# Kernel tuning notes

Hardware: AMD Instinct MI355X
Metric: run time of the kernel (lower is better)

## Reference

```python
import jax, jax.numpy as jnp
import numpy as np

HEADS, DIM_HEAD = 8, 64  # per init_kwargs


def cdist(x, w):
    """Euclidean distance between rows of x [..., n, d] and w [m, d] -> [..., n, m].
    Matches torch.cdist (non-squared) / L2DistanceLinear(squared=False)."""
    sq = (x * x).sum(-1, keepdims=True) + (w * w).sum(-1) - 2.0 * (x @ w.T)
    return jnp.sqrt(jnp.maximum(sq, 0.0))


def setup_inputs() -> dict:
    key = jax.random.key(0)
    k1, k2, k3 = jax.random.split(key, 3)
    B, N, D = 4, 2048, 512
    dim_inner = HEADS * DIM_HEAD  # 512
    x = jax.random.normal(k1, (B, N, D), dtype=jnp.float32)
    w_qkv = jax.random.normal(k2, (3 * dim_inner, D), dtype=jnp.float32)
    w_out = jax.random.normal(k3, (D, dim_inner), dtype=jnp.float32)
    return {"x": x, "w_qkv": w_qkv, "w_out": w_out}


def reference(x, w_qkv, w_out):
    B, N, D = x.shape
    scale = DIM_HEAD ** -0.5

    # L2-distance QKV projection (cdist, non-squared, no negate/bias)
    qkv = cdist(x, w_qkv)                                  # [B, N, 3*H*DH]
    qkv = qkv.reshape(B, N, 3, HEADS, DIM_HEAD).transpose(2, 0, 3, 1, 4)  # [3, B, H, N, DH]
    q, k, v = qkv[0], qkv[1], qkv[2]

    # neg squared-L2 attention scores: -(||q||^2 + ||k||^2 - 2 q.k)
    q_sq = (q * q).sum(-1)                                 # [B, H, N]
    k_sq = (k * k).sum(-1)                                 # [B, H, N]
    dots = jnp.einsum('bhid,bhjd->bhij', q, k)             # [B, H, N, N]
    sim = -(q_sq[..., :, None] + k_sq[..., None, :] - 2.0 * dots) * scale

    attn = jax.nn.softmax(sim, axis=-1)
    out = jnp.einsum('bhij,bhjd->bhid', attn, v)           # [B, H, N, DH]
    out = out.transpose(0, 2, 1, 3).reshape(B, N, HEADS * DIM_HEAD)

    # L2-distance output projection
    return cdist(out, w_out)                               # [B, N, D]
```

## Files before the change

kernel.cpp:

```cpp
#include <hip/hip_runtime.h>
#include <stdint.h>

typedef float v4f  __attribute__((ext_vector_type(4)));
typedef float v16f __attribute__((ext_vector_type(16)));
typedef short v8s  __attribute__((ext_vector_type(8)));
typedef uint32_t u32;

#define DEVI static __device__ __forceinline__

DEVI unsigned short f2bf(float f) {
    u32 u = __builtin_bit_cast(u32, f);
    u = (u + 0x7fffu + ((u >> 16) & 1u)) >> 16;
    return (unsigned short)u;
}
DEVI float bf2f(unsigned short h) {
    u32 u = ((u32)h) << 16;
    return __builtin_bit_cast(float, u);
}

DEVI float fexp2(float x) {
#if __has_builtin(__builtin_amdgcn_exp2f)
    return __builtin_amdgcn_exp2f(x);
#else
    float r;
    asm("v_exp_f32 %0, %1" : "=v"(r) : "v"(x));
    return r;
#endif
}

template <typename T>
DEVI void async16(const T* g, T* l) {
    __builtin_amdgcn_global_load_lds(
        (const __attribute__((address_space(1))) u32*)g,
        (__attribute__((address_space(3))) u32*)l, 16, 0, 0);
}

DEVI v4f bmfma(v8s a, v8s b, v4f c) {
    return __builtin_amdgcn_mfma_f32_16x16x32_bf16(a, b, c, 0, 0, 0);
}
DEVI v16f bmfma32(v8s a, v8s b, v16f c) {
    return __builtin_amdgcn_mfma_f32_32x32x16_bf16(a, b, c, 0, 0, 0);
}

#if __has_builtin(__builtin_amdgcn_permlane32_swap)
#define HAVE_PLSWAP 1
typedef unsigned int v2u __attribute__((ext_vector_type(2)));
#endif

DEVI void swap32(u32 a, u32 b, u32& lo, u32& hi) {
#ifdef HAVE_PLSWAP
    v2u r = __builtin_amdgcn_permlane32_swap(a, b, false, false);
    lo = r.x; hi = r.y;
#else
    u32 ax = __shfl_xor(a, 32), bx = __shfl_xor(b, 32);
    int hh = (threadIdx.x & 63) >> 5;
    lo = hh ? bx : a;
    hi = hh ? b : ax;
#endif
}

static const size_t HSZ = 32ull * 2048 * 64;

__launch_bounds__(256, 2)
__global__ void prep_all(const float* __restrict__ X, const float* __restrict__ WQ,
                         const float* __restrict__ WO,
                         unsigned short* __restrict__ Xb, unsigned short* __restrict__ WQb,
                         unsigned short* __restrict__ WOb,
                         float* __restrict__ xsq, float* __restrict__ wqsq,
                         float* __restrict__ wosq, float* __restrict__ wors)
{
    const int bid = blockIdx.x;
    const int w = threadIdx.x >> 6, lane = threadIdx.x & 63;
    const float* src; unsigned short* dst; float* Sq; float* Rs = nullptr;
    int r;
    if (bid < 2048)      { src = X;  dst = Xb;  Sq = xsq;  r = bid * 4 + w; }
    else if (bid < 2432) { src = WQ; dst = WQb; Sq = wqsq; r = (bid - 2048) * 4 + w; }
    else                 { src = WO; dst = WOb; Sq = wosq; Rs = wors; r = (bid - 2432) * 4 + w; }

    const float* xr = src + (size_t)r * 512 + lane * 8;
    float4 a = *(const float4*)xr;
    float4 c = *(const float4*)(xr + 4);
    float s = a.x*a.x + a.y*a.y + a.z*a.z + a.w*a.w
            + c.x*c.x + c.y*c.y + c.z*c.z + c.w*c.w;
    float sm = a.x + a.y + a.z + a.w + c.x + c.y + c.z + c.w;
    uint4 pkv;
    unsigned short* e = (unsigned short*)&pkv;
    e[0] = f2bf(a.x); e[1] = f2bf(a.y); e[2] = f2bf(a.z); e[3] = f2bf(a.w);
    e[4] = f2bf(c.x); e[5] = f2bf(c.y); e[6] = f2bf(c.z); e[7] = f2bf(c.w);
    *(uint4*)(dst + (size_t)r * 512 + lane * 8) = pkv;
#pragma unroll
    for (int d = 32; d > 0; d >>= 1) {
        s  += __shfl_xor(s, d);
        sm += __shfl_xor(sm, d);
    }
    if (lane == 0) { Sq[r] = s; if (Rs) Rs[r] = sm; }
}

__launch_bounds__(256, 2)
__global__ void gemm_cdist(const unsigned short* __restrict__ A,
                           const unsigned short* __restrict__ B,
                           const float* __restrict__ Asq,
                           const float* __restrict__ Bsq,
                           unsigned short* __restrict__ QKV,
                           float* __restrict__ Ksqc)
{
    __shared__ unsigned short lsm[4 * 8192];
    const int t = threadIdx.x;
    const int lane = t & 63, w = t >> 6;
    const int low = lane & 15, quad = lane >> 4;
    const int wm = w & 1, wn = w >> 1;
    const int tM = blockIdx.x * 128, tN = blockIdx.y * 128;

    v4f acc[4][4];
#pragma unroll
    for (int a = 0; a < 4; ++a)
#pragma unroll
        for (int b = 0; b < 4; ++b) acc[a][b] = (v4f){0.f, 0.f, 0.f, 0.f};

    int kstage = 0;
    auto STAGE = [&](int buf) {
        unsigned short* lA = lsm + buf * 8192;
        unsigned short* lB = lA + 4096;
#pragma unroll
        for (int is = 0; is < 2; ++is) {
            int slot = is * 256 + t;
            int r = slot >> 2, bp = slot & 3, bs = bp ^ (r & 3);
            async16(A + (size_t)(tM + r) * 512 + kstage + bs * 8, lA + slot * 8);
            async16(B + (size_t)(tN + r) * 512 + kstage + bs * 8, lB + slot * 8);
        }
        kstage += 32;
    };

    STAGE(0);
    STAGE(1);

#pragma unroll
    for (int iter = 0; iter < 16; ++iter) {
        if (iter <= 13) STAGE((iter + 2) & 3);
        if (iter <= 13)      asm volatile("s_waitcnt vmcnt(8)" ::: "memory");
        else if (iter == 14) asm volatile("s_waitcnt vmcnt(4)" ::: "memory");
        else                 asm volatile("s_waitcnt vmcnt(0)" ::: "memory");
        __builtin_amdgcn_s_barrier();
        __builtin_amdgcn_sched_barrier(0);

        const unsigned short* lA = lsm + (iter & 3) * 8192;
        const unsigned short* lB = lA + 4096;

        v8s bfr[4];
#pragma unroll
        for (int ns = 0; ns < 4; ++ns) {
            int row = wn * 64 + ns * 16 + low;
            bfr[ns] = *(const v8s*)(lB + (row * 4 + (quad ^ (row & 3))) * 8);
        }
#pragma unroll
        for (int ms = 0; ms < 4; ++ms) {
            int row = wm * 64 + ms * 16 + low;
            v8s af = *(const v8s*)(lA + (row * 4 + (quad ^ (row & 3))) * 8);
#pragma unroll
            for (int ns = 0; ns < 4; ++ns)
                acc[ms][ns] = bmfma(af, bfr[ns], acc[ms][ns]);
        }
    }

    const int tt = tN >> 9;
    if (tt != 2) {
#pragma unroll
        for (int ms = 0; ms < 4; ++ms) {
#pragma unroll
            for (int reg = 0; reg < 4; ++reg) {
                const int row = tM + wm * 64 + ms * 16 + quad * 4 + reg;
                const int b = row >> 11, i = row & 2047;
                float kacc = 0.f;
#pragma unroll
                for (int ns = 0; ns < 4; ++ns) {
                    const int col = tN + wn * 64 + ns * 16 + low;
                    float dot = acc[ms][ns][reg];
                    float val = sqrtf(fmaxf(Asq[row] + Bsq[col] - 2.f * dot, 0.f)) - 32.f;
                    int h = (col >> 6) & 7, d = col & 63, bh = b * 8 + h;
                    if (tt == 0) {
                        QKV[((size_t)bh * 2048 + i) * 64 + d] =
                            f2bf(val * 0.36067376022224085f);
                    } else {
                        QKV[HSZ + ((size_t)bh * 2048 + i) * 64 + d] = f2bf(val);
                        kacc += val * val;
                    }
                }
                if (tt == 1) {
#pragma unroll
                    for (int d = 1; d < 16; d <<= 1) kacc += __shfl_xor(kacc, d);
                    if (low == 0) {
                        int h = ((tN + wn * 64) >> 6) & 7;
                        Ksqc[(size_t)(b * 8 + h) * 2048 + i] = -kacc * 0.18033688011112042f;
                    }
                }
            }
        }
    } else {
        u32 packed[4][4][2];
#pragma unroll
        for (int ms = 0; ms < 4; ++ms)
#pragma unroll
            for (int ns = 0; ns < 4; ++ns) {
                const int col = tN + wn * 64 + ns * 16 + low;
                float bs_ = Bsq[col];
#pragma unroll
                for (int rp = 0; rp < 2; ++rp) {
                    u32 pk = 0;
#pragma unroll
                    for (int sub = 0; sub < 2; ++sub) {
                        int reg = rp * 2 + sub;
                        int row = tM + wm * 64 + ms * 16 + quad * 4 + reg;
                        float val = sqrtf(fmaxf(Asq[row] + bs_
                                                - 2.f * acc[ms][ns][reg], 0.f)) - 32.f;
                        pk |= (u32)f2bf(val) << (16 * sub);
                    }
                    packed[ms][ns][rp] = pk;
                }
            }
        u32* lT32 = (u32*)lsm;
#pragma unroll
        for (int p = 0; p < 2; ++p) {
            __syncthreads();
            if (wm == p) {
#pragma unroll
                for (int ms = 0; ms < 4; ++ms)
#pragma unroll
                    for (int ns = 0; ns < 4; ++ns) {
                        int cl = wn * 64 + ns * 16 + low;
#pragma unroll
                        for (int rp = 0; rp < 2; ++rp)
                            lT32[cl * 36 + ms * 8 + quad * 2 + rp] = packed[ms][ns][rp];
                    }
            }
            __syncthreads();
#pragma unroll
            for (int cc = 0; cc < 4; ++cc) {
                int col = cc * 32 + (t >> 3);
                int i0 = (t & 7) * 8;
                uint4 vvv = *(const uint4*)(lsm + col * 72 + i0);
                int colg = tN + col;
                int h = (colg >> 6) & 7, d = colg & 63;
                int rowg = tM + p * 64 + i0;
                int b = rowg >> 11, i = rowg & 2047;
                *(uint4*)(QKV + 2 * HSZ
                          + ((size_t)((b * 8 + h) * 64 + d)) * 2048 + i) = vvv;
            }
        }
    }
    (void)0;
}

__launch_bounds__(256, 2)
__global__ void flash_attn(const unsigned short* __restrict__ Q,
                           const unsigned short* __restrict__ K,
                           const unsigned short* __restrict__ VT,
                           const float* __restrict__ Ksqc,
                           unsigned short* __restrict__ OP,
                           float* __restrict__ Osqp)
{
    __shared__ unsigned short lK[4][64 * 64];
    __shared__ unsigned short lV[4][64 * 64];
    __shared__ float lKqA[2048];
    const int t = threadIdx.x, lane = t & 63, w = t >> 6;
    const int i31 = lane & 31, h = lane >> 5;
    const int bid = blockIdx.x;
    const int bh = (bid & 7) * 4 + (bid >> 7);
    const int qt = (bid >> 3) & 15;
    const size_t base = (size_t)bh * (2048 * 64);
    const int row0 = qt * 128 + w * 32;

    v8s qfr[4];
#pragma unroll
    for (int kt = 0; kt < 4; ++kt)
        qfr[kt] = *(const v8s*)(Q + base + (size_t)(row0 + i31) * 64 + kt * 16 + h * 8);

    v16f o[2];
    float lacc = 0.f;
#pragma unroll
    for (int dt = 0; dt < 2; ++dt)
#pragma unroll
        for (int r = 0; r < 16; ++r) o[dt][r] = 0.f;

    const unsigned short* kg = K + base;
    const unsigned short* vg = VT + (size_t)bh * 64 * 2048;
    const float* kqg = Ksqc + (size_t)bh * 2048;

    auto STAGE = [&](int buf) {
#pragma unroll
        for (int is = 0; is < 2; ++is) {
            int slot = is * 256 + t;
            int r = slot >> 3, bp = slot & 7, bs = bp ^ (r & 7);
            async16(kg + (size_t)r * 64 + bs * 8, &lK[buf][slot * 8]);
        }
#pragma unroll
        for (int is = 0; is < 2; ++is) {
            int slot = is * 256 + t;
            int r = slot >> 3, bp = slot & 7, bs = bp ^ (r & 7);
            async16(vg + (size_t)r * 2048 + bs * 8, &lV[buf][slot * 8]);
        }
        kg += 64 * 64; vg += 64;
    };

    auto COMPUTE = [&](int cb, int kqoff) {
        const int jrow0 = i31, jrow1 = 32 + i31;
        v8s kf0[4], kf1[4];
#pragma unroll
        for (int kt = 0; kt < 4; ++kt) {
            kf0[kt] = *(const v8s*)(&lK[cb][(jrow0 * 8 + ((2 * kt + h) ^ (jrow0 & 7))) * 8]);
            kf1[kt] = *(const v8s*)(&lK[cb][(jrow1 * 8 + ((2 * kt + h) ^ (jrow1 & 7))) * 8]);
        }
        v16f sa0, sa1;
#pragma unroll
        for (int r1 = 0; r1 < 4; ++r1) {
            v4f kq0 = *(const v4f*)(&lKqA[kqoff + r1 * 8 + h * 4]);
            v4f kq1 = *(const v4f*)(&lKqA[kqoff + 32 + r1 * 8 + h * 4]);
#pragma unroll
            for (int u = 0; u < 4; ++u) {
                sa0[4 * r1 + u] = kq0[u];
                sa1[4 * r1 + u] = kq1[u];
            }
        }
#pragma unroll
        for (int kt = 0; kt < 4; ++kt) sa0 = bmfma32(kf0[kt], qfr[kt], sa0);
#pragma unroll
        for (int kt = 0; kt < 4; ++kt) sa1 = bmfma32(kf1[kt], qfr[kt], sa1);

        u32 pk0[8];
#pragma unroll
        for (int r1 = 0; r1 < 4; ++r1) {
            float p0 = fexp2(sa0[4 * r1 + 0]);
            float p1 = fexp2(sa0[4 * r1 + 1]);
            float p2 = fexp2(sa0[4 * r1 + 2]);
            float p3 = fexp2(sa0[4 * r1 + 3]);
            lacc += (p0 + p1) + (p2 + p3);
            pk0[2 * r1] = __builtin_amdgcn_perm(
                __builtin_bit_cast(u32, p1), __builtin_bit_cast(u32, p0),
                0x07060302u);
            pk0[2 * r1 + 1] = __builtin_amdgcn_perm(
                __builtin_bit_cast(u32, p3), __builtin_bit_cast(u32, p2),
                0x07060302u);
        }
#pragma unroll
        for (int c2 = 0; c2 < 2; ++c2) {
            const int jb = 2 * c2;
            v8s vf[2];
#pragma unroll
            for (int dt = 0; dt < 2; ++dt) {
                const int drow = dt * 32 + i31;
                vf[dt] = *(const v8s*)(&lV[cb][(drow * 8 + ((jb + h) ^ (drow & 7))) * 8]);
            }
            uint4 dd;
            swap32(pk0[4 * c2 + 0], pk0[4 * c2 + 2], dd.x, dd.z);
            swap32(pk0[4 * c2 + 1], pk0[4 * c2 + 3], dd.y, dd.w);
            v8s af = __builtin_bit_cast(v8s, dd);
            o[0] = bmfma32(af, vf[0], o[0]);
            o[1] = bmfma32(af, vf[1], o[1]);
        }

        u32 pk1[8];
#pragma unroll
        for (int r1 = 0; r1 < 4; ++r1) {
            float p0 = fexp2(sa1[4 * r1 + 0]);
            float p1 = fexp2(sa1[4 * r1 + 1]);
            float p2 = fexp2(sa1[4 * r1 + 2]);
            float p3 = fexp2(sa1[4 * r1 + 3]);
            lacc += (p0 + p1) + (p2 + p3);
            pk1[2 * r1] = __builtin_amdgcn_perm(
                __builtin_bit_cast(u32, p1), __builtin_bit_cast(u32, p0),
                0x07060302u);
            pk1[2 * r1 + 1] = __builtin_amdgcn_perm(
                __builtin_bit_cast(u32, p3), __builtin_bit_cast(u32, p2),
                0x07060302u);
        }
#pragma unroll
        for (int c2 = 0; c2 < 2; ++c2) {
            const int jb = 4 + 2 * c2;
            v8s vf[2];
#pragma unroll
            for (int dt = 0; dt < 2; ++dt) {
                const int drow = dt * 32 + i31;
                vf[dt] = *(const v8s*)(&lV[cb][(drow * 8 + ((jb + h) ^ (drow & 7))) * 8]);
            }
            uint4 dd;
            swap32(pk1[4 * c2 + 0], pk1[4 * c2 + 2], dd.x, dd.z);
            swap32(pk1[4 * c2 + 1], pk1[4 * c2 + 3], dd.y, dd.w);
            v8s af = __builtin_bit_cast(v8s, dd);
            o[0] = bmfma32(af, vf[0], o[0]);
            o[1] = bmfma32(af, vf[1], o[1]);
        }
    };

#pragma unroll
    for (int is = 0; is < 2; ++is) {
        int slot = is * 256 + t;
        async16(kqg + slot * 4, lKqA + slot * 4);
    }
    STAGE(0);
    STAGE(1);

#pragma unroll 1
    for (int g = 0; g < 7; ++g) {
#pragma unroll
        for (int u = 0; u < 4; ++u) {
            STAGE((u + 2) & 3);
            asm volatile("s_waitcnt vmcnt(8)" ::: "memory");
            __builtin_amdgcn_s_barrier();
            __builtin_amdgcn_sched_barrier(0);
            COMPUTE(u, (g * 4 + u) * 64);
        }
    }
    STAGE(2);
    asm volatile("s_waitcnt vmcnt(8)" ::: "memory");
    __builtin_amdgcn_s_barrier();
    __builtin_amdgcn_sched_barrier(0);
    COMPUTE(0, 28 * 64);
    STAGE(3);
    asm volatile("s_waitcnt vmcnt(8)" ::: "memory");
    __builtin_amdgcn_s_barrier();
    __builtin_amdgcn_sched_barrier(0);
    COMPUTE(1, 29 * 64);
    asm volatile("s_waitcnt vmcnt(4)" ::: "memory");
    __builtin_amdgcn_s_barrier();
    __builtin_amdgcn_sched_barrier(0);
    COMPUTE(2, 30 * 64);
    asm volatile("s_waitcnt vmcnt(0)" ::: "memory");
    __builtin_amdgcn_s_barrier();
    __builtin_amdgcn_sched_barrier(0);
    COMPUTE(3, 31 * 64);

    const int b = bh >> 3, hh = bh & 7;
    lacc += __shfl_xor(lacc, 32);
    unsigned short* ob = OP + ((size_t)(b * 2048 + row0)) * 512 + hh * 64;
    float* osq = Osqp + (size_t)hh * 8192 + b * 2048 + row0;
#pragma unroll
    for (int r = 0; r < 16; ++r) {
        const int rl = (r & 3) + 8 * (r >> 2) + 4 * h;
        float inv = 1.f / __shfl(lacc, rl);
        unsigned short e0 = f2bf(o[0][r] * inv);
        unsigned short e1 = f2bf(o[1][r] * inv);
        ob[(size_t)rl * 512 + i31] = e0;
        ob[(size_t)rl * 512 + 32 + i31] = e1;
        float f0 = bf2f(e0) + 32.f, f1 = bf2f(e1) + 32.f;
        float s = f0 * f0 + f1 * f1;
        s += __shfl_xor(s, 1);  s += __shfl_xor(s, 2);  s += __shfl_xor(s, 4);
        s += __shfl_xor(s, 8);  s += __shfl_xor(s, 16);
        if (i31 == 0) osq[rl] = s;
    }
}

__launch_bounds__(256, 2)
__global__ void gemm_out(const unsigned short* __restrict__ A,
                         const unsigned short* __restrict__ B,
                         const float* __restrict__ Osqp,
                         const float* __restrict__ Bsq,
                         const float* __restrict__ Brs,
                         float* __restrict__ OUT)
{
    __shared__ unsigned short lA[2][128 * 64];
    __shared__ unsigned short lB[2][64 * 64];
    __shared__ float lAsq[128];
    const int t = threadIdx.x;
    const int lane = t & 63, w = t >> 6;
    const int low = lane & 15, quad = lane >> 4;
    const int wm = w & 1, wn = w >> 1;
    const int tM = blockIdx.x * 128, tN = blockIdx.y * 64;

    if (t < 128) {
        float s = 0.f;
#pragma unroll
        for (int hh = 0; hh < 8; ++hh) s += Osqp[(size_t)hh * 8192 + tM + t];
        lAsq[t] = s;
    }

    v4f acc[4][2];
#pragma unroll
    for (int a = 0; a < 4; ++a)
#pragma unroll
        for (int b = 0; b < 2; ++b) acc[a][b] = (v4f){0.f, 0.f, 0.f, 0.f};

    int kstage = 0;
    auto STAGE = [&](int buf) {
#pragma unroll
        for (int is = 0; is < 4; ++is) {
            int slot = is * 256 + t;
            int r = slot >> 3, bp = slot & 7, bs = bp ^ (r & 7);
            async16(A + (size_t)(tM + r) * 512 + kstage + bs * 8, &lA[buf][slot * 8]);
        }
#pragma unroll
        for (int is = 0; is < 2; ++is) {
            int slot = is * 256 + t;
            int r = slot >> 3, bp = slot & 7, bs = bp ^ (r & 7);
            async16(B + (size_t)(tN + r) * 512 + kstage + bs * 8, &lB[buf][slot * 8]);
        }
        kstage += 64;
    };

    STAGE(0);
    __syncthreads();

#pragma unroll 2
    for (int iter = 0; iter < 8; ++iter) {
        const int c = iter & 1;
        if (iter < 7) STAGE(1 - c);

        v8s bfr[2][2];
#pragma unroll
        for (int ns = 0; ns < 2; ++ns) {
            int row = wn * 32 + ns * 16 + low;
#pragma unroll
            for (int kc = 0; kc < 2; ++kc)
                bfr[ns][kc] = *(const v8s*)(&lB[c][(row * 8 + ((kc * 4 + quad) ^ (row & 7))) * 8]);
        }
#pragma unroll
        for (int ms = 0; ms < 4; ++ms) {
            int row = wm * 64 + ms * 16 + low;
            v8s af0 = *(const v8s*)(&lA[c][(row * 8 + ((0 + quad) ^ (row & 7))) * 8]);
            v8s af1 = *(const v8s*)(&lA[c][(row * 8 + ((4 + quad) ^ (row & 7))) * 8]);
#pragma unroll
            for (int ns = 0; ns < 2; ++ns) {
                acc[ms][ns] = bmfma(af0, bfr[ns][0], acc[ms][ns]);
                acc[ms][ns] = bmfma(af1, bfr[ns][1], acc[ms][ns]);
            }
        }
        __syncthreads();
    }

#pragma unroll
    for (int ms = 0; ms < 4; ++ms) {
#pragma unroll
        for (int ns = 0; ns < 2; ++ns) {
#pragma unroll
            for (int reg = 0; reg < 4; ++reg) {
                int rloc = wm * 64 + ms * 16 + quad * 4 + reg;
                int row = tM + rloc;
                int col = tN + wn * 32 + ns * 16 + low;
                float val = sqrtf(fmaxf(lAsq[rloc] + Bsq[col]
                                        - 2.f * (acc[ms][ns][reg] + 32.f * Brs[col]), 0.f));
                OUT[(size_t)row * 512 + col] = val;
            }
        }
    }
}

extern "C" void kernel_launch(void* const* d_in, const int* in_sizes, int n_in,
                              void* d_out, int out_size, void* d_ws, size_t ws_size,
                              hipStream_t stream)
{
    const float* x    = (const float*)d_in[0];
    const float* wqkv = (const float*)d_in[1];
    const float* wout = (const float*)d_in[2];
    float* out = (float*)d_out;

    char* ws = (char*)d_ws;
    size_t off = 0;
    auto alloc = [&](size_t bytes) -> void* {
        void* p = ws + off;
        off += (bytes + 255) & ~(size_t)255;
        return p;
    };
    unsigned short* xb   = (unsigned short*)alloc(8192ull * 512 * 2);
    unsigned short* wqb  = (unsigned short*)alloc(1536ull * 512 * 2);
    unsigned short* wob  = (unsigned short*)alloc(512ull * 512 * 2);
    unsigned short* qkv  = (unsigned short*)alloc(3ull * HSZ * 2);
    unsigned short* outp = (unsigned short*)alloc(8192ull * 512 * 2);
    float* xsq  = (float*)alloc(8192 * 4);
    float* wqsq = (float*)alloc(1536 * 4);
    float* wosq = (float*)alloc(512 * 4);
    float* wors = (float*)alloc(512 * 4);
    float* ksqc = (float*)alloc(65536ull * 4);
    float* osqp = (float*)alloc(8ull * 8192 * 4);

    prep_all<<<2560, 256, 0, stream>>>(x, wqkv, wout, xb, wqb, wob,
                                       xsq, wqsq, wosq, wors);

    gemm_cdist<<<dim3(64, 12), 256, 0, stream>>>(xb, wqb, xsq, wqsq, qkv, ksqc);
    flash_attn<<<512, 256, 0, stream>>>(qkv, qkv + HSZ, qkv + 2 * HSZ,
                                        ksqc, outp, osqp);
    gemm_out<<<dim3(64, 8), 256, 0, stream>>>(outp, wob, osqp, wosq, wors, out);
}
```

Measured before the change: 160.2 us.

## Use three-stage LDS ring with single barrier in both cdist GEMMs

The QKV GEMM drops from a 4-deep to a 3-deep LDS ring (prefetch distance 1 instead of 2), cutting shared memory per block. The output GEMM moves from double-buffered 64-wide K chunks with two __syncthreads per step to a 3-buffer ring of 32-wide chunks. It waits on partial vmcnt and uses one barrier per iteration. The aim is to lower LDS use and synchronisation cost, at the risk of exposing more global-load latency with the shallower prefetch.

```diff
diff --git a/kernel.cpp b/kernel.cpp
--- a/kernel.cpp
+++ b/kernel.cpp
@@ -104,7 +104,7 @@
                            unsigned short* __restrict__ QKV,
                            float* __restrict__ Ksqc)
 {
-    __shared__ unsigned short lsm[4 * 8192];
+    __shared__ unsigned short lsm[3 * 8192];
     const int t = threadIdx.x;
     const int lane = t & 63, w = t >> 6;
     const int low = lane & 15, quad = lane >> 4;
@@ -132,18 +132,19 @@
     };
 
     STAGE(0);
-    STAGE(1);
 
 #pragma unroll
     for (int iter = 0; iter < 16; ++iter) {
-        if (iter <= 13) STAGE((iter + 2) & 3);
-        if (iter <= 13)      asm volatile("s_waitcnt vmcnt(8)" ::: "memory");
-        else if (iter == 14) asm volatile("s_waitcnt vmcnt(4)" ::: "memory");
-        else                 asm volatile("s_waitcnt vmcnt(0)" ::: "memory");
+        if (iter < 15) {
+            STAGE((iter + 1) % 3);
+            asm volatile("s_waitcnt vmcnt(4)" ::: "memory");
+        } else {
+            asm volatile("s_waitcnt vmcnt(0)" ::: "memory");
+        }
         __builtin_amdgcn_s_barrier();
         __builtin_amdgcn_sched_barrier(0);
 
-        const unsigned short* lA = lsm + (iter & 3) * 8192;
+        const unsigned short* lA = lsm + (iter % 3) * 8192;
         const unsigned short* lB = lA + 4096;
 
         v8s bfr[4];
@@ -456,8 +457,7 @@
                          const float* __restrict__ Brs,
                          float* __restrict__ OUT)
 {
-    __shared__ unsigned short lA[2][128 * 64];
-    __shared__ unsigned short lB[2][64 * 64];
+    __shared__ unsigned short lsm[3 * 6144];
     __shared__ float lAsq[128];
     const int t = threadIdx.x;
     const int lane = t & 63, w = t >> 6;
@@ -480,49 +480,52 @@
 
     int kstage = 0;
     auto STAGE = [&](int buf) {
-#pragma unroll
-        for (int is = 0; is < 4; ++is) {
-            int slot = is * 256 + t;
-            int r = slot >> 3, bp = slot & 7, bs = bp ^ (r & 7);
-            async16(A + (size_t)(tM + r) * 512 + kstage + bs * 8, &lA[buf][slot * 8]);
-        }
+        unsigned short* lA = lsm + buf * 6144;
+        unsigned short* lB = lA + 4096;
 #pragma unroll
         for (int is = 0; is < 2; ++is) {
             int slot = is * 256 + t;
-            int r = slot >> 3, bp = slot & 7, bs = bp ^ (r & 7);
-            async16(B + (size_t)(tN + r) * 512 + kstage + bs * 8, &lB[buf][slot * 8]);
-        }
-        kstage += 64;
+            int r = slot >> 2, bp = slot & 3, bs = bp ^ (r & 3);
+            async16(A + (size_t)(tM + r) * 512 + kstage + bs * 8, lA + slot * 8);
+        }
+        {
+            int slot = t;
+            int r = slot >> 2, bp = slot & 3, bs = bp ^ (r & 3);
+            async16(B + (size_t)(tN + r) * 512 + kstage + bs * 8, lB + slot * 8);
+        }
+        kstage += 32;
     };
 
     STAGE(0);
-    __syncthreads();
-
-#pragma unroll 2
-    for (int iter = 0; iter < 8; ++iter) {
-        const int c = iter & 1;
-        if (iter < 7) STAGE(1 - c);
-
-        v8s bfr[2][2];
+
+#pragma unroll
+    for (int iter = 0; iter < 16; ++iter) {
+        if (iter < 15) {
+            STAGE((iter + 1) % 3);
+            asm volatile("s_waitcnt vmcnt(3)" ::: "memory");
+        } else {
+            asm volatile("s_waitcnt vmcnt(0)" ::: "memory");
+        }
+        __builtin_amdgcn_s_barrier();
+        __builtin_amdgcn_sched_barrier(0);
+
+        const unsigned short* lA = lsm + (iter % 3) * 6144;
+        const unsigned short* lB = lA + 4096;
+
+        v8s bfr[2];
 #pragma unroll
         for (int ns = 0; ns < 2; ++ns) {
             int row = wn * 32 + ns * 16 + low;
-#pragma unroll
-            for (int kc = 0; kc < 2; ++kc)
-                bfr[ns][kc] = *(const v8s*)(&lB[c][(row * 8 + ((kc * 4 + quad) ^ (row & 7))) * 8]);
+            bfr[ns] = *(const v8s*)(lB + (row * 4 + (quad ^ (row & 3))) * 8);
         }
 #pragma unroll
         for (int ms = 0; ms < 4; ++ms) {
             int row = wm * 64 + ms * 16 + low;
-            v8s af0 = *(const v8s*)(&lA[c][(row * 8 + ((0 + quad) ^ (row & 7))) * 8]);
-            v8s af1 = *(const v8s*)(&lA[c][(row * 8 + ((4 + quad) ^ (row & 7))) * 8]);
-#pragma unroll
-            for (int ns = 0; ns < 2; ++ns) {
-                acc[ms][ns] = bmfma(af0, bfr[ns][0], acc[ms][ns]);
-                acc[ms][ns] = bmfma(af1, bfr[ns][1], acc[ms][ns]);
-            }
-        }
-        __syncthreads();
+            v8s af = *(const v8s*)(lA + (row * 4 + (quad ^ (row & 3))) * 8);
+#pragma unroll
+            for (int ns = 0; ns < 2; ++ns)
+                acc[ms][ns] = bmfma(af, bfr[ns], acc[ms][ns]);
+        }
     }
 
 #pragma unroll
```

Result: faster. 156.0 us (-2.6%).
